# Kernel tuning notes

Hardware: AMD Instinct MI355X
Metric: run time of the kernel (lower is better)

## Reference

```python
import jax, jax.numpy as jnp
import numpy as np

B, T_H, T_F = 8192, 128, 125
MOTION_DIM, H = 6, 128


def setup_inputs() -> dict:
    key = jax.random.key(0)
    ks = jax.random.split(key, 24)
    s = 1.0 / np.sqrt(H)  # torch LSTM/Linear default init scale

    def p(k, shape):
        return jax.random.uniform(k, shape, jnp.float32, -s, s)

    inp = {"hist": jax.random.normal(ks[0], (B, T_H, MOTION_DIM), jnp.float32)}
    i = 1
    for pre, in0 in (("enc", MOTION_DIM), ("dec", 2)):
        for l, ind in enumerate((in0, H)):
            inp[f"{pre}_Wih{l}"] = p(ks[i], (4 * H, ind)); i += 1
            inp[f"{pre}_Whh{l}"] = p(ks[i], (4 * H, H)); i += 1
            inp[f"{pre}_bih{l}"] = p(ks[i], (4 * H,)); i += 1
            inp[f"{pre}_bhh{l}"] = p(ks[i], (4 * H,)); i += 1
    inp["head_W1"] = p(ks[i], (128, H)); i += 1
    inp["head_b1"] = p(ks[i], (128,)); i += 1
    inp["head_W2"] = p(ks[i], (2, 128)); i += 1
    inp["head_b2"] = p(ks[i], (2,)); i += 1
    return inp


def _cell(x, h, c, Wih, Whh, bih, bhh):
    # PyTorch LSTM gate order: i, f, g, o
    gates = x @ Wih.T + h @ Whh.T + (bih + bhh)
    i, f, g, o = jnp.split(gates, 4, axis=-1)
    c = jax.nn.sigmoid(f) * c + jax.nn.sigmoid(i) * jnp.tanh(g)
    h = jax.nn.sigmoid(o) * jnpp_tanh(c) if False else jax.nn.sigmoid(o) * jnp.tanh(c)
    return h, c


def reference(hist,
              enc_Wih0, enc_Whh0, enc_bih0, enc_bhh0,
              enc_Wih1, enc_Whh1, enc_bih1, enc_bhh1,
              dec_Wih0, dec_Whh0, dec_bih0, dec_bhh0,
              dec_Wih1, dec_Whh1, dec_bih1, dec_bhh1,
              head_W1, head_b1, head_W2, head_b2):
    b = hist.shape[0]
    z = jnp.zeros((b, H), hist.dtype)

    # ---- encoder: 2-layer LSTM over hist, keep only final (h, c) ----
    def enc_step(carry, x_t):
        h0, c0, h1, c1 = carry
        h0, c0 = _cell(x_t, h0, c0, enc_Wih0, enc_Whh0, enc_bih0, enc_bhh0)
        h1, c1 = _cell(h0, h1, c1, enc_Wih1, enc_Whh1, enc_bih1, enc_bhh1)
        return (h0, c0, h1, c1), None

    (h0, c0, h1, c1), _ = jax.lax.scan(
        enc_step, (z, z, z, z), jnp.swapaxes(hist, 0, 1))  # [T_h, B, 6]

    last_pos = hist[:, -1, :2]

    def dec_step(carry, _):
        h0, c0, h1, c1, x = carry
        h0, c0 = _cell(x, h0, c0, dec_Wih0, dec_Whh0, dec_bih0, dec_bhh0)
        h1, c1 = _cell(h0, h1, c1, dec_Wih1, dec_Whh1, dec_bih1, dec_bhh1)
        nxt = jax.nn.relu(h1 @ head_W1.T + head_b1) @ head_W2.T + head_b2
        return (h0, c0, h1, c1, nxt), nxt

    _, preds = jax.lax.scan(dec_step, (h0, c0, h1, c1, last_pos), None,
                            length=T_F)
    return jnp.swapaxes(preds, 0, 1)  # [B, T_f, 2]
```

## Files before the change

### kernel.cpp

```cpp
#include <hip/hip_runtime.h>


typedef _Float16 f16;
typedef _Float16 f16x4 __attribute__((ext_vector_type(4)));
typedef _Float16 f16x8 __attribute__((ext_vector_type(8)));
typedef float    f32x4 __attribute__((ext_vector_type(4)));

#define MFMA16(a,b,c) __builtin_amdgcn_mfma_f32_16x16x32_f16((a),(b),(c),0,0,0)

#define BM 32
#define NBLK 256
#define PACE_TGT 32

#define HOFF_E0 0
#define HOFF_E1 81920
#define HOFF_D0 212992
#define HOFF_D1 294912
#define HOFF_H  425984
#define H_TOTAL 442368
#define FOFF    221184
#define FB_E0 0
#define FB_E1 512
#define FB_D0 1024
#define FB_D1 1536
#define FB_H1 2048
#define FB_W2 2176
#define FB_B2 2432
#define F_TOTAL 2434
#define BAR_F   2560
#define BAR_BYTES 8192

#define HS 140
#define XS 36
#define O1S 133

#define HBUF 4480
#define XBUF 1152
#define L_H0H 0
#define L_H0L 8960
#define L_H1H 17920
#define L_H1L 26880
#define L_XH  35840
#define L_XL  38144
#define L_HALVES 40448
#define LDS_BYTES 97920

__device__ __forceinline__ float fsig(float x){ return 1.0f/(1.0f+__expf(-x)); }
__device__ __forceinline__ float ftanh(float x){
  float a = fabsf(x);
  float e = __expf(-2.0f*a);
  float t = (1.0f-e)/(1.0f+e);
  return x < 0.0f ? -t : t;
}

__device__ __forceinline__ void grid_pace(unsigned* __restrict__ bar, int idx, int g, int tid){
  __syncthreads();
  if (tid == 0){
    unsigned* p = &bar[idx*8 + g];
    __hip_atomic_fetch_add(p, 1u, __ATOMIC_RELAXED, __HIP_MEMORY_SCOPE_AGENT);
    while (__hip_atomic_load(p, __ATOMIC_RELAXED, __HIP_MEMORY_SCOPE_AGENT) < (unsigned)PACE_TGT)
      __builtin_amdgcn_s_sleep(1);
  }
  __syncthreads();
}

template<int STRIDE>
__device__ __forceinline__ f16x8 load_afrag(const f16* buf, int m, int kc, int lane){
  const f16* p = buf + (m*16 + (lane&15))*STRIDE + kc + ((lane>>4)<<2);
  f16x4 lo = *(const f16x4*)p;
  f16x4 hi = *(const f16x4*)(p+16);
  return __builtin_shufflevector(lo, hi, 0,1,2,3,4,5,6,7);
}

__device__ __forceinline__ void init_acc(f32x4 acc[2][4],
                                         const float* __restrict__ bias, int wv, int lane){
#pragma unroll
  for (int i=0;i<4;++i){
    float bv = bias[wv*64 + i*16 + (lane&15)];
    f32x4 b4 = {bv,bv,bv,bv};
    acc[0][i]=b4; acc[1][i]=b4;
  }
}

template<int KT, int SPLIT, int SB>
__device__ __forceinline__ void gemm2(f32x4 acc[2][4],
    const f16x8* __restrict__ Bp,
    const f16* __restrict__ Ah, const f16* __restrict__ Al,
    const f16* __restrict__ Ch, const f16* __restrict__ Cl,
    int wv, int lane)
{
  const int nb = wv*4;
  f16x8 Bc[4], Bn[4];
#pragma unroll
  for (int i=0;i<4;++i) Bc[i] = Bp[(nb + i)*64 + lane];
#pragma unroll
  for (int kt=0; kt<KT; ++kt){
    if (kt+1 < KT){
#pragma unroll
      for (int i=0;i<4;++i) Bn[i] = Bp[((kt+1)*32 + nb + i)*64 + lane];
    }
    f16x8 a0h,a0l,a1h,a1l;
    if (kt < SPLIT){
      int kc = kt*32;
      a0h = load_afrag<HS>(Ah, 0, kc, lane);
      a0l = load_afrag<HS>(Al, 0, kc, lane);
      a1h = load_afrag<HS>(Ah, 1, kc, lane);
      a1l = load_afrag<HS>(Al, 1, kc, lane);
    } else {
      int kc = (kt-SPLIT)*32;
      a0h = load_afrag<SB>(Ch, 0, kc, lane);
      a0l = load_afrag<SB>(Cl, 0, kc, lane);
      a1h = load_afrag<SB>(Ch, 1, kc, lane);
      a1l = load_afrag<SB>(Cl, 1, kc, lane);
    }
#pragma unroll
    for (int i=0;i<4;++i){
      acc[0][i] = MFMA16(a0h, Bc[i], acc[0][i]);
      acc[1][i] = MFMA16(a1h, Bc[i], acc[1][i]);
      acc[0][i] = MFMA16(a0l, Bc[i], acc[0][i]);
      acc[1][i] = MFMA16(a1l, Bc[i], acc[1][i]);
    }
#pragma unroll
    for (int i=0;i<4;++i) Bc[i] = Bn[i];
  }
}

__device__ __forceinline__ void quad_transpose(float&a0,float&a1,float&a2,float&a3,int q){
  bool odd = (q & 1) != 0;
  float s0 = odd ? a0 : a1, s1 = odd ? a2 : a3;
  float r0 = __shfl_xor(s0,1), r1 = __shfl_xor(s1,1);
  float b0 = odd ? r0 : a0, b1 = odd ? a1 : r0;
  float b2 = odd ? r1 : a2, b3 = odd ? a3 : r1;
  bool hi = (q & 2) != 0;
  float u0 = hi ? b0 : b2, u1 = hi ? b1 : b3;
  float v0 = __shfl_xor(u0,2), v1 = __shfl_xor(u1,2);
  a0 = hi ? v0 : b0; a1 = hi ? v1 : b1;
  a2 = hi ? b2 : v0; a3 = hi ? b3 : v1;
}

__device__ __forceinline__ void lstm_update_m(f32x4 acc[2][4], float cr[2][4],
    f16* __restrict__ Dh, f16* __restrict__ Dl, int wv, int lane)
{
  const int q = lane & 3;
  const int rsub = ((lane>>4)<<2) + q;
  const int usub = wv*16 + ((lane&15)>>2);
#pragma unroll
  for (int mt=0;mt<2;++mt)
#pragma unroll
  for (int nt=0;nt<4;++nt){
    float a0=acc[mt][nt][0], a1=acc[mt][nt][1], a2=acc[mt][nt][2], a3=acc[mt][nt][3];
    quad_transpose(a0,a1,a2,a3,q);
    float iv=fsig(a0), fv=fsig(a1), gv=ftanh(a2), ov=fsig(a3);
    float cn = fv*cr[mt][nt] + iv*gv;
    cr[mt][nt] = cn;
    float h = ov*ftanh(cn);
    f16 hh = (f16)h;
    f16 hl = (f16)(h - (float)hh);
    int off = (mt*16 + rsub)*HS + usub + nt*4;
    Dh[off]=hh; Dl[off]=hl;
  }
}

__global__ void __launch_bounds__(512, 2)
lstm_main(const float* __restrict__ hist, float* __restrict__ ws,
          float* __restrict__ out)
{
  const f16* wh = (const f16*)ws;
  const float* wf = ws + FOFF;
  unsigned* bar = (unsigned*)(ws + FOFF + BAR_F);
  const f16x8* BE0 = (const f16x8*)(wh + HOFF_E0);
  const f16x8* BE1 = (const f16x8*)(wh + HOFF_E1);
  const f16x8* BD0 = (const f16x8*)(wh + HOFF_D0);
  const f16x8* BD1 = (const f16x8*)(wh + HOFF_D1);
  const f16x8* BH  = (const f16x8*)(wh + HOFF_H);

  extern __shared__ __align__(16) f16 smem[];
  float* o1buf = (float*)(smem + L_HALVES);

  const int tid  = threadIdx.x;
  const int wv   = tid >> 6;
  const int lane = tid & 63;
  const int b0   = blockIdx.x * BM;
  const int g    = blockIdx.x & 7;
  const int lidx = lane & 15;

  for (int i = tid; i < L_HALVES; i += 512) smem[i] = (f16)0.f;
  float c0r[2][4] = {{0,0,0,0},{0,0,0,0}};
  float c1r[2][4] = {{0,0,0,0},{0,0,0,0}};
  f32x4 acc[2][4];

  const int lr = tid/6, ld = tid - (tid/6)*6;

  __syncthreads();
  if (tid < 192){
    float v = hist[(b0+lr)*768 + ld];
    f16 hv = (f16)v;
    smem[L_XH + XBUF + lr*XS + ld] = hv;
    smem[L_XL + XBUF + lr*XS + ld] = (f16)(v - (float)hv);
  }
  __syncthreads();

  for (int t=0; t<128; ++t){
    const int c  = t & 1;
    const int hw = c*HBUF, hr = (c^1)*HBUF;
    const int xw = c*XBUF, xr = (c^1)*XBUF;

    init_acc(acc, wf + FB_E0, wv, lane);
    gemm2<5,4,XS>(acc, BE0,
                  smem + L_H0H + hr, smem + L_H0L + hr,
                  smem + L_XH  + xr, smem + L_XL  + xr, wv, lane);
    if (t < 127 && tid < 192){
      float v = hist[(b0+lr)*768 + (t+1)*6 + ld];
      f16 hv = (f16)v;
      smem[L_XH + xw + lr*XS + ld] = hv;
      smem[L_XL + xw + lr*XS + ld] = (f16)(v - (float)hv);
    }
    lstm_update_m(acc, c0r, smem + L_H0H + hw, smem + L_H0L + hw, wv, lane);
    __syncthreads();

    init_acc(acc, wf + FB_E1, wv, lane);
    gemm2<8,4,HS>(acc, BE1,
                  smem + L_H0H + hw, smem + L_H0L + hw,
                  smem + L_H1H + hr, smem + L_H1L + hr, wv, lane);
    lstm_update_m(acc, c1r, smem + L_H1H + hw, smem + L_H1L + hw, wv, lane);
    grid_pace(bar, t, g, tid);
  }

  if (tid < 64){
    int r = tid>>1, j = tid&1;
    float v = hist[(b0+r)*768 + 762 + j];
    f16 hv = (f16)v;
    smem[L_XH + XBUF + r*XS + j] = hv;
    smem[L_XL + XBUF + r*XS + j] = (f16)(v - (float)hv);
  }
  __syncthreads();

  for (int t=0; t<125; ++t){
    const int c  = t & 1;
    const int hw = c*HBUF, hr = (c^1)*HBUF;
    const int xw = c*XBUF, xr = (c^1)*XBUF;

    init_acc(acc, wf + FB_D0, wv, lane);
    gemm2<5,4,XS>(acc, BD0,
                  smem + L_H0H + hr, smem + L_H0L + hr,
                  smem + L_XH  + xr, smem + L_XL  + xr, wv, lane);
    lstm_update_m(acc, c0r, smem + L_H0H + hw, smem + L_H0L + hw, wv, lane);
    __syncthreads();

    init_acc(acc, wf + FB_D1, wv, lane);
    gemm2<8,4,HS>(acc, BD1,
                  smem + L_H0H + hw, smem + L_H0L + hw,
                  smem + L_H1H + hr, smem + L_H1L + hr, wv, lane);
    lstm_update_m(acc, c1r, smem + L_H1H + hw, smem + L_H1L + hw, wv, lane);
    __syncthreads();

    {
      const f16* h1wH = smem + L_H1H + hw;
      const f16* h1wL = smem + L_H1L + hw;
      float bH1 = wf[FB_H1 + wv*16 + lidx];
      f32x4 ha0 = {bH1,bH1,bH1,bH1};
      f32x4 ha1 = ha0;
#pragma unroll
      for (int kt=0;kt<4;++kt){
        f16x8 Wc = BH[(kt*8 + wv)*64 + lane];
        int kc = kt*32;
        f16x8 a0h = load_afrag<HS>(h1wH, 0, kc, lane);
        f16x8 a0l = load_afrag<HS>(h1wL, 0, kc, lane);
        f16x8 a1h = load_afrag<HS>(h1wH, 1, kc, lane);
        f16x8 a1l = load_afrag<HS>(h1wL, 1, kc, lane);
        ha0 = MFMA16(a0h, Wc, ha0);
        ha0 = MFMA16(a0l, Wc, ha0);
        ha1 = MFMA16(a1h, Wc, ha1);
        ha1 = MFMA16(a1l, Wc, ha1);
      }
#pragma unroll
      for (int r=0;r<4;++r){
        float v0 = ha0[r]; v0 = v0 > 0.f ? v0 : 0.f;
        float v1 = ha1[r]; v1 = v1 > 0.f ? v1 : 0.f;
        int rr = ((lane>>4)<<2) + r;
        o1buf[rr*O1S      + wv*16 + lidx] = v0;
        o1buf[(16+rr)*O1S + wv*16 + lidx] = v1;
      }
    }
    __syncthreads();

    if (tid < 64){
      int r = tid>>1, j = tid&1;
      const float* op = o1buf + r*O1S;
      const float* w2 = wf + FB_W2 + j;
      float s0=0.f,s1=0.f,s2=0.f,s3=0.f;
#pragma unroll
      for (int k=0;k<128;k+=4){
        s0 = fmaf(op[k],   w2[2*k],   s0);
        s1 = fmaf(op[k+1], w2[2*k+2], s1);
        s2 = fmaf(op[k+2], w2[2*k+4], s2);
        s3 = fmaf(op[k+3], w2[2*k+6], s3);
      }
      float pred = wf[FB_B2 + j] + ((s0+s1)+(s2+s3));
      out[(b0+r)*250 + t*2 + j] = pred;
      f16 ph = (f16)pred;
      smem[L_XH + xw + r*XS + j] = ph;
      smem[L_XL + xw + r*XS + j] = (f16)(pred - (float)ph);
    }
    grid_pace(bar, 128 + t, g, tid);
  }
}

__global__ void setup_kernel(
    const float* __restrict__ eWih0, const float* __restrict__ eWhh0,
    const float* __restrict__ ebih0, const float* __restrict__ ebhh0,
    const float* __restrict__ eWih1, const float* __restrict__ eWhh1,
    const float* __restrict__ ebih1, const float* __restrict__ ebhh1,
    const float* __restrict__ dWih0, const float* __restrict__ dWhh0,
    const float* __restrict__ dbih0, const float* __restrict__ dbhh0,
    const float* __restrict__ dWih1, const float* __restrict__ dWhh1,
    const float* __restrict__ dbih1, const float* __restrict__ dbhh1,
    const float* __restrict__ W1, const float* __restrict__ b1,
    const float* __restrict__ W2, const float* __restrict__ b2,
    float* __restrict__ ws)
{
  int i = blockIdx.x*256 + threadIdx.x;
  if (i < H_TOTAL){
    f16* whp = (f16*)ws;
    const float *Wa, *Wb; int ka, kb, off; bool head = false;
    if      (i < HOFF_E1){ off=HOFF_E0; Wa=eWhh0; ka=128; Wb=eWih0; kb=6; }
    else if (i < HOFF_D0){ off=HOFF_E1; Wa=eWih1; ka=128; Wb=eWhh1; kb=128; }
    else if (i < HOFF_D1){ off=HOFF_D0; Wa=dWhh0; ka=128; Wb=dWih0; kb=2; }
    else if (i < HOFF_H) { off=HOFF_D1; Wa=dWih1; ka=128; Wb=dWhh1; kb=128; }
    else                 { off=HOFF_H;  Wa=W1; ka=128; Wb=W1; kb=0; head=true; }
    int local = i - off;
    int j     = local & 7;
    int lane  = (local>>3) & 63;
    int nk    = local >> 9;
    int NTl   = head ? 8 : 32;
    int n     = nk % NTl;
    int kt    = nk / NTl;
    int col   = n*16 + (lane&15);
    int koff  = ((j>>2)<<4) + ((lane>>4)<<2) + (j&3);
    int kin   = kt*32 + koff;
    float val;
    if (head){
      val = (kin < 128) ? W1[col*128 + kin] : 0.f;
    } else {
      int orow = (col&3)*128 + (col>>2);
      val = (kin < ka) ? Wa[orow*ka + kin]
          : ((kin < ka+kb) ? Wb[orow*kb + (kin-ka)] : 0.f);
    }
    whp[i] = (f16)val;
  } else if (i < H_TOTAL + F_TOTAL){
    int f = i - H_TOTAL;
    float* wfp = ws + FOFF;
    if (f < 2048){
      int layer = f >> 9, c = f & 511;
      int orow = (c&3)*128 + (c>>2);
      const float *bi, *bh;
      if      (layer==0){ bi=ebih0; bh=ebhh0; }
      else if (layer==1){ bi=ebih1; bh=ebhh1; }
      else if (layer==2){ bi=dbih0; bh=dbhh0; }
      else              { bi=dbih1; bh=dbhh1; }
      wfp[f] = bi[orow] + bh[orow];
    } else if (f < 2176){
      wfp[f] = b1[f-2048];
    } else if (f < 2432){
      int k = (f-2176)>>1, j = (f-2176)&1;
      wfp[f] = W2[j*128 + k];
    } else {
      wfp[f] = b2[f-2432];
    }
  }
}

extern "C" void kernel_launch(void* const* d_in, const int* in_sizes, int n_in,
                              void* d_out, int out_size, void* d_ws, size_t ws_size,
                              hipStream_t stream)
{
  const float* hist = (const float*)d_in[0];
  float* ws = (float*)d_ws;

  (void)hipFuncSetAttribute(reinterpret_cast<const void*>(lstm_main),
                            hipFuncAttributeMaxDynamicSharedMemorySize, LDS_BYTES);

  (void)hipMemsetAsync((char*)d_ws + (size_t)(FOFF + BAR_F)*4, 0, BAR_BYTES, stream);

  int total = H_TOTAL + F_TOTAL;
  setup_kernel<<<(total + 255)/256, 256, 0, stream>>>(
      (const float*)d_in[1],  (const float*)d_in[2],
      (const float*)d_in[3],  (const float*)d_in[4],
      (const float*)d_in[5],  (const float*)d_in[6],
      (const float*)d_in[7],  (const float*)d_in[8],
      (const float*)d_in[9],  (const float*)d_in[10],
      (const float*)d_in[11], (const float*)d_in[12],
      (const float*)d_in[13], (const float*)d_in[14],
      (const float*)d_in[15], (const float*)d_in[16],
      (const float*)d_in[17], (const float*)d_in[18],
      (const float*)d_in[19], (const float*)d_in[20],
      ws);

  lstm_main<<<NBLK, 512, LDS_BYTES, stream>>>(hist, ws, (float*)d_out);
}
```

Baseline: 3.254 ms.

## Drop cross-block pacing barrier and parallelize final head dot product across all threads

Removes the per-timestep grid pacing atomics (groups of 32 blocks spinning on a global counter) and replaces them with plain block-level __syncthreads, along with the memset of the barrier area. The pacing had been keeping blocks in lockstep, presumably to share weights in L2. The second head layer now spreads each 128-long dot product over 8 threads with shuffle reduction instead of one thread, cutting the serial tail per step. Without pacing, blocks may drift apart and reuse cached weights less.

```diff
diff --git a/kernel.cpp b/kernel.cpp
--- a/kernel.cpp
+++ b/kernel.cpp
@@ -10,7 +10,6 @@
 
 #define BM 32
 #define NBLK 256
-#define PACE_TGT 32
 
 #define HOFF_E0 0
 #define HOFF_E1 81920
@@ -27,8 +26,6 @@
 #define FB_W2 2176
 #define FB_B2 2432
 #define F_TOTAL 2434
-#define BAR_F   2560
-#define BAR_BYTES 8192
 
 #define HS 140
 #define XS 36
@@ -51,17 +48,6 @@
   float e = __expf(-2.0f*a);
   float t = (1.0f-e)/(1.0f+e);
   return x < 0.0f ? -t : t;
-}
-
-__device__ __forceinline__ void grid_pace(unsigned* __restrict__ bar, int idx, int g, int tid){
-  __syncthreads();
-  if (tid == 0){
-    unsigned* p = &bar[idx*8 + g];
-    __hip_atomic_fetch_add(p, 1u, __ATOMIC_RELAXED, __HIP_MEMORY_SCOPE_AGENT);
-    while (__hip_atomic_load(p, __ATOMIC_RELAXED, __HIP_MEMORY_SCOPE_AGENT) < (unsigned)PACE_TGT)
-      __builtin_amdgcn_s_sleep(1);
-  }
-  __syncthreads();
 }
 
 template<int STRIDE>
@@ -167,7 +153,6 @@
 {
   const f16* wh = (const f16*)ws;
   const float* wf = ws + FOFF;
-  unsigned* bar = (unsigned*)(ws + FOFF + BAR_F);
   const f16x8* BE0 = (const f16x8*)(wh + HOFF_E0);
   const f16x8* BE1 = (const f16x8*)(wh + HOFF_E1);
   const f16x8* BD0 = (const f16x8*)(wh + HOFF_D0);
@@ -181,7 +166,6 @@
   const int wv   = tid >> 6;
   const int lane = tid & 63;
   const int b0   = blockIdx.x * BM;
-  const int g    = blockIdx.x & 7;
   const int lidx = lane & 15;
 
   for (int i = tid; i < L_HALVES; i += 512) smem[i] = (f16)0.f;
@@ -223,7 +207,7 @@
                   smem + L_H0H + hw, smem + L_H0L + hw,
                   smem + L_H1H + hr, smem + L_H1L + hr, wv, lane);
     lstm_update_m(acc, c1r, smem + L_H1H + hw, smem + L_H1L + hw, wv, lane);
-    grid_pace(bar, t, g, tid);
+    __syncthreads();
   }
 
   if (tid < 64){
@@ -284,25 +268,33 @@
     }
     __syncthreads();
 
-    if (tid < 64){
-      int r = tid>>1, j = tid&1;
-      const float* op = o1buf + r*O1S;
-      const float* w2 = wf + FB_W2 + j;
-      float s0=0.f,s1=0.f,s2=0.f,s3=0.f;
-#pragma unroll
-      for (int k=0;k<128;k+=4){
-        s0 = fmaf(op[k],   w2[2*k],   s0);
-        s1 = fmaf(op[k+1], w2[2*k+2], s1);
-        s2 = fmaf(op[k+2], w2[2*k+4], s2);
-        s3 = fmaf(op[k+3], w2[2*k+6], s3);
+    {
+      const int r = tid >> 4;
+      const int j = (tid >> 3) & 1;
+      const int s = tid & 7;
+      const float* op = o1buf + r*O1S + s*16;
+      const float* w2 = wf + FB_W2 + s*32 + j;
+      float p0=0.f,p1=0.f,p2=0.f,p3=0.f;
+#pragma unroll
+      for (int i=0;i<16;i+=4){
+        p0 = fmaf(op[i],   w2[2*i],   p0);
+        p1 = fmaf(op[i+1], w2[2*i+2], p1);
+        p2 = fmaf(op[i+2], w2[2*i+4], p2);
+        p3 = fmaf(op[i+3], w2[2*i+6], p3);
       }
-      float pred = wf[FB_B2 + j] + ((s0+s1)+(s2+s3));
-      out[(b0+r)*250 + t*2 + j] = pred;
-      f16 ph = (f16)pred;
-      smem[L_XH + xw + r*XS + j] = ph;
-      smem[L_XL + xw + r*XS + j] = (f16)(pred - (float)ph);
-    }
-    grid_pace(bar, 128 + t, g, tid);
+      float p = (p0+p1)+(p2+p3);
+      p += __shfl_xor(p, 1);
+      p += __shfl_xor(p, 2);
+      p += __shfl_xor(p, 4);
+      if (s == 0){
+        float pred = wf[FB_B2 + j] + p;
+        out[(b0+r)*250 + t*2 + j] = pred;
+        f16 ph = (f16)pred;
+        smem[L_XH + xw + r*XS + j] = ph;
+        smem[L_XL + xw + r*XS + j] = (f16)(pred - (float)ph);
+      }
+    }
+    __syncthreads();
   }
 }
 
@@ -380,8 +372,6 @@
   (void)hipFuncSetAttribute(reinterpret_cast<const void*>(lstm_main),
                             hipFuncAttributeMaxDynamicSharedMemorySize, LDS_BYTES);
 
-  (void)hipMemsetAsync((char*)d_ws + (size_t)(FOFF + BAR_F)*4, 0, BAR_BYTES, stream);
-
   int total = H_TOTAL + F_TOTAL;
   setup_kernel<<<(total + 255)/256, 256, 0, stream>>>(
       (const float*)d_in[1],  (const float*)d_in[2],
```

Result: slower. 4.425 ms, median of 2 (+36.0%).
